# Kernel optimization log

Hardware: AMD Instinct MI355X
Metric: run time of the kernel (lower is better)

## Reference

```python
import jax, jax.numpy as jnp
import numpy as np

NUM_HEADS = 16
NUM_FEATURES = 1024
HEAD_DIM = NUM_FEATURES // NUM_HEADS
MAX_WAVELENGTH = 10000.0
SCALE_FACTOR = 1.0


def apply_rope(x, positions):
    # x: [B, S, H, D], positions: [B, S]
    half = HEAD_DIM // 2
    fraction = 2.0 * jnp.arange(half, dtype=x.dtype) / HEAD_DIM
    timescale = MAX_WAVELENGTH ** fraction                      # [half]
    sinusoid = positions[..., None].astype(x.dtype) / timescale  # [B, S, half]
    sinusoid = sinusoid[..., None, :] / SCALE_FACTOR             # [B, S, 1, half]
    sin, cos = jnp.sin(sinusoid), jnp.cos(sinusoid)
    x1, x2 = jnp.split(x, 2, axis=-1)
    return jnp.concatenate([x1 * cos - x2 * sin, x2 * cos + x1 * sin], axis=-1).astype(x.dtype)


def setup_inputs() -> dict:
    key = jax.random.key(0)
    ks = jax.random.split(key, 9)
    B, S, F = 2, 2048, NUM_FEATURES
    std = 1.0 / np.sqrt(F)
    inp = {
        "x": jax.random.normal(ks[0], (B, S, F), dtype=jnp.float32),
        "positions": jnp.broadcast_to(jnp.arange(S, dtype=jnp.int32), (B, S)),
        "Wq": jax.random.normal(ks[1], (F, F), dtype=jnp.float32) * std,
        "bq": jnp.zeros((F,), dtype=jnp.float32),
        "Wk": jax.random.normal(ks[2], (F, F), dtype=jnp.float32) * std,
        "bk": jnp.zeros((F,), dtype=jnp.float32),
        "Wv": jax.random.normal(ks[3], (F, F), dtype=jnp.float32) * std,
        "bv": jnp.zeros((F,), dtype=jnp.float32),
        "Wo": jax.random.normal(ks[4], (F, F), dtype=jnp.float32) * std,
        "bo": jnp.zeros((F,), dtype=jnp.float32),
    }
    return inp


def reference(x, positions, Wq, bq, Wk, bk, Wv, bv, Wo, bo):
    B, S, F = x.shape
    H, D = NUM_HEADS, HEAD_DIM
    q = (x @ Wq + bq).reshape(B, S, H, D)
    k = (x @ Wk + bk).reshape(B, S, H, D)
    v = (x @ Wv + bv).reshape(B, S, H, D)
    q = apply_rope(q, positions)
    k = apply_rope(k, positions)
    scale = jnp.sqrt(jnp.asarray(D, dtype=x.dtype))
    # scores: [B, H, S, S]
    scores = jnp.einsum("bqhd,bkhd->bhqk", q, k) / scale
    causal = jnp.tril(jnp.ones((S, S), dtype=bool))
    big_neg = jnp.finfo(scores.dtype).min
    scores = jnp.where(causal, scores, big_neg)
    attn = jax.nn.softmax(scores, axis=-1)
    out = jnp.einsum("bhqk,bkhd->bqhd", attn, v).reshape(B, S, F)
    return out @ Wo + bo
```

## Files before the change

kernel.cpp:

```cpp
#include <hip/hip_runtime.h>
#include <hip/hip_bf16.h>

#define S_LEN 2048
#define NF 1024
#define NH 16
#define HD 64
#define NB 2
#define M_TOT 4096

typedef __bf16 bf16x8 __attribute__((ext_vector_type(8)));
typedef float f32x4 __attribute__((ext_vector_type(4)));
typedef unsigned short u16;

__device__ __forceinline__ u16 f2bf(float f) {
  union { float f; unsigned u; } v; v.f = f;
  unsigned r = v.u + 0x7FFFu + ((v.u >> 16) & 1u);
  return (u16)(r >> 16);
}

__device__ __forceinline__ unsigned pk2bf(float a, float b) {
  __hip_bfloat162 t = __float22bfloat162_rn(make_float2(a, b));
  union { __hip_bfloat162 h; unsigned u; } u; u.h = t; return u.u;
}

__device__ __forceinline__ f32x4 mfma16(bf16x8 a, bf16x8 b, f32x4 c) {
  return __builtin_amdgcn_mfma_f32_16x16x32_bf16(a, b, c, 0, 0, 0);
}

__device__ __forceinline__ void gll16(const u16* g, u16* l) {
  __builtin_amdgcn_global_load_lds(
      (const __attribute__((address_space(1))) unsigned int*)g,
      (__attribute__((address_space(3))) unsigned int*)l, 16, 0, 0);
}

__device__ __forceinline__ u16* swz(u16* base, int row, int chunk) {
  return (u16*)((char*)base + row * 128 + ((chunk ^ (row & 7)) * 16));
}
__device__ __forceinline__ const u16* swz(const u16* base, int row, int chunk) {
  return (const u16*)((const char*)base + row * 128 + ((chunk ^ (row & 7)) * 16));
}

__global__ void __launch_bounds__(256) prep_kernel(
    const float* __restrict__ x, u16* __restrict__ xb,
    const int* __restrict__ positions, float2* __restrict__ rtab,
    const float* __restrict__ W0, const float* __restrict__ W1,
    const float* __restrict__ W2, const float* __restrict__ W3,
    u16* __restrict__ T0, u16* __restrict__ T1,
    u16* __restrict__ T2, u16* __restrict__ T3) {
  __shared__ float t[32][33];
  const int bx = blockIdx.x, tid = threadIdx.x;
  if (bx < 4096) {
    int i = (bx * 256 + tid) * 4;
    float4 v = *(const float4*)(x + i);
    ushort4 o;
    o.x = f2bf(v.x); o.y = f2bf(v.y); o.z = f2bf(v.z); o.w = f2bf(v.w);
    *(ushort4*)(xb + i) = o;
  } else if (bx < 4608) {
    int idx = (bx - 4096) * 256 + tid;
    int p = idx & 31;
    int bs = idx >> 5;
    float pos = (float)positions[bs];
    float ang = pos / __powf(10000.0f, (float)p * (1.0f / 32.0f));
    float sn, cs;
    sincosf(ang, &sn, &cs);
    rtab[idx] = make_float2(sn, cs);
  } else {
    int idx = bx - 4608;
    int z = idx >> 10, rem = idx & 1023;
    const float* W = (z == 0) ? W0 : (z == 1) ? W1 : (z == 2) ? W2 : W3;
    u16* Wt = (z == 0) ? T0 : (z == 1) ? T1 : (z == 2) ? T2 : T3;
    int n0 = (rem & 31) * 32, k0 = (rem >> 5) * 32;
    int tx = tid & 31, ty0 = tid >> 5;
#pragma unroll
    for (int i = 0; i < 4; i++) {
      int ty = ty0 + i * 8;
      t[ty][tx] = W[(size_t)(k0 + ty) * NF + n0 + tx];
    }
    __syncthreads();
#pragma unroll
    for (int i = 0; i < 4; i++) {
      int ty = ty0 + i * 8;
      Wt[(size_t)(n0 + ty) * NF + k0 + tx] = f2bf(t[tx][ty]);
    }
  }
}

__device__ __forceinline__ void mm_core(const u16* __restrict__ A, const u16* __restrict__ Bt,
                                        int m0, int n0, int kstart,
                                        u16* As, u16* Bs, f32x4 acc[4][4]) {
  const int tid = threadIdx.x;
  const int lane = tid & 63, w = tid >> 6;
  const int l15 = lane & 15, quad = lane >> 4;
  const int wr = w >> 1, wc = w & 1;
#pragma unroll
  for (int i = 0; i < 4; i++)
#pragma unroll
    for (int j = 0; j < 4; j++) {
      f32x4 z = {0.f, 0.f, 0.f, 0.f};
      acc[i][j] = z;
    }
  const u16* gA[4];
  const u16* gB[4];
#pragma unroll
  for (int i = 0; i < 4; i++) {
    int ci = i * 256 + tid;
    int row = ci >> 3, col = (ci & 7) ^ (row & 7);
    gA[i] = &A[(size_t)(m0 + row) * NF + col * 8];
    gB[i] = &Bt[(size_t)(n0 + row) * NF + col * 8];
  }
  for (int s = 0; s < NF / 64; s++) {
    const int k0 = ((s + kstart) & (NF / 64 - 1)) * 64;
    __syncthreads();
#pragma unroll
    for (int i = 0; i < 4; i++) {
      gll16(gA[i] + k0, &As[(i * 256 + w * 64) * 8]);
      gll16(gB[i] + k0, &Bs[(i * 256 + w * 64) * 8]);
    }
    __syncthreads();
#pragma unroll
    for (int kk = 0; kk < 2; kk++) {
      bf16x8 af[4], bfr[4];
#pragma unroll
      for (int i = 0; i < 4; i++)
        af[i] = *(const bf16x8*)swz(As, wr * 64 + i * 16 + l15, kk * 4 + quad);
#pragma unroll
      for (int j = 0; j < 4; j++)
        bfr[j] = *(const bf16x8*)swz(Bs, wc * 64 + j * 16 + l15, kk * 4 + quad);
#pragma unroll
      for (int i = 0; i < 4; i++)
#pragma unroll
        for (int j = 0; j < 4; j++)
          acc[i][j] = mfma16(af[i], bfr[j], acc[i][j]);
    }
  }
}

#define QSCL 0.18033688f

__global__ void __launch_bounds__(256) gemm_qkv_kernel(
    const u16* __restrict__ xb,
    const u16* __restrict__ wtq, const u16* __restrict__ wtk, const u16* __restrict__ wtv,
    const float* __restrict__ bq, const float* __restrict__ bk, const float* __restrict__ bv,
    const float2* __restrict__ rtab,
    u16* __restrict__ qo, u16* __restrict__ ko, u16* __restrict__ vto) {
  __shared__ u16 As[128 * 64], Bs[128 * 64];
  const int bx = blockIdx.x;
  const int xcd = bx & 7, slot = bx >> 3;
  const int z = slot >> 5, intra = slot & 31;
  const int by = (xcd >> 1) * 8 + (intra >> 2);
  const int bxn = (xcd & 1) * 4 + (intra & 3);
  const int kstart = (intra * 3 + z * 5) & 15;
  const u16* Wt = (z == 0) ? wtq : (z == 1) ? wtk : wtv;
  const float* bias = (z == 0) ? bq : (z == 1) ? bk : bv;
  const int m0 = by * 128, n0 = bxn * 128;
  f32x4 acc[4][4];
  mm_core(xb, Wt, m0, n0, kstart, As, Bs, acc);
  const int tid = threadIdx.x;
  const int lane = tid & 63, w = tid >> 6;
  const int l15 = lane & 15, quad = lane >> 4;
  const int wr = w >> 1, wc = w & 1;
  if (z < 2) {
    u16* out = (z == 0) ? qo : ko;
    const float oscl = (z == 0) ? QSCL : 1.0f;
#pragma unroll
    for (int i = 0; i < 4; i++) {
#pragma unroll
      for (int r = 0; r < 4; r++) {
        int gm = m0 + wr * 64 + i * 16 + quad * 4 + r;
        int b = gm >> 11, s = gm & 2047;
#pragma unroll
        for (int j = 0; j < 2; j++) {
          int col1 = n0 + wc * 64 + j * 16 + l15;
          int p = j * 16 + l15;
          float2 sc = rtab[gm * 32 + p];
          float x1 = acc[i][j][r] + bias[col1];
          float x2 = acc[i][j + 2][r] + bias[col1 + 32];
          float o1 = (x1 * sc.y - x2 * sc.x) * oscl;
          float o2 = (x2 * sc.y + x1 * sc.x) * oscl;
          int h = col1 >> 6;
          size_t base = ((size_t)((b * NH + h) * S_LEN + s)) * HD;
          out[base + p] = f2bf(o1);
          out[base + p + 32] = f2bf(o2);
        }
      }
    }
  } else {
#pragma unroll
    for (int i = 0; i < 4; i++) {
      int gm0 = m0 + wr * 64 + i * 16 + quad * 4;
      int b = gm0 >> 11, s0 = gm0 & 2047;
#pragma unroll
      for (int j = 0; j < 4; j++) {
        int col = n0 + wc * 64 + j * 16 + l15;
        int h = col >> 6, d = col & 63;
        float bb = bias[col];
        ushort4 pk;
        pk.x = f2bf(acc[i][j][0] + bb);
        pk.y = f2bf(acc[i][j][1] + bb);
        pk.z = f2bf(acc[i][j][2] + bb);
        pk.w = f2bf(acc[i][j][3] + bb);
        *(ushort4*)&vto[((size_t)((b * NH + h) * HD + d)) * S_LEN + s0] = pk;
      }
    }
  }
}

__global__ void __launch_bounds__(256) gemm_o_kernel(const u16* __restrict__ ab,
                                                     const u16* __restrict__ wto,
                                                     const float* __restrict__ bo,
                                                     float* __restrict__ out) {
  __shared__ u16 As[128 * 64], Bs[128 * 64];
  const int bxr = blockIdx.x;
  const int xcd = bxr & 7, intra = bxr >> 3;
  const int by = (xcd >> 1) * 8 + (intra >> 2);
  const int bxn = (xcd & 1) * 4 + (intra & 3);
  const int kstart = (intra * 3) & 15;
  const int m0 = by * 128, n0 = bxn * 128;
  f32x4 acc[4][4];
  mm_core(ab, wto, m0, n0, kstart, As, Bs, acc);
  const int tid = threadIdx.x;
  const int lane = tid & 63, w = tid >> 6;
  const int l15 = lane & 15, quad = lane >> 4;
  const int wr = w >> 1, wc = w & 1;
#pragma unroll
  for (int i = 0; i < 4; i++) {
#pragma unroll
    for (int j = 0; j < 4; j++) {
      int col = n0 + wc * 64 + j * 16 + l15;
      float bb = bo[col];
#pragma unroll
      for (int r = 0; r < 4; r++) {
        int gm = m0 + wr * 64 + i * 16 + quad * 4 + r;
        out[(size_t)gm * NF + col] = acc[i][j][r] + bb;
      }
    }
  }
}

__global__ void __launch_bounds__(256) attn_kernel(
    const u16* __restrict__ qb, const u16* __restrict__ kb,
    const u16* __restrict__ vtb, u16* __restrict__ ob) {
  __shared__ u16 ks[2 * 64 * 64];
  __shared__ u16 vs[2 * 64 * 64];
  __shared__ u16 ps[4][16 * 64];
  const int bx = blockIdx.x;
  const int qt = (bx < 512) ? (31 - (bx >> 5)) : ((bx - 512) >> 5);
  const int bh = bx & 31;
  const int tid = threadIdx.x;
  const int lane = tid & 63, w = tid >> 6, l15 = lane & 15, quad = lane >> 4;
  const int bb = bh >> 4, h = bh & 15;
  const size_t kvbase = (size_t)bh * S_LEN;
  const size_t vbase = (size_t)bh * HD;
  const int Q0 = qt * 64;
  const int nit = qt + 1;
  const int r0 = tid >> 3, c0 = tid & 7;
  const int r1 = r0 + 32;

  bf16x8 ones;
#pragma unroll
  for (int i = 0; i < 8; i++) ones[i] = (__bf16)1.0f;

  bf16x8 qf[2];
  {
    const u16* qrow = &qb[(kvbase + Q0 + w * 16 + l15) * HD];
#pragma unroll
    for (int hh = 0; hh < 2; hh++)
      qf[hh] = *(const bf16x8*)&qrow[hh * 32 + quad * 8];
  }

  float mrun = -1e30f;
  f32x4 Oa[4], lacc;
  { f32x4 z = {0.f, 0.f, 0.f, 0.f}; lacc = z;
#pragma unroll
    for (int t = 0; t < 4; t++) Oa[t] = z; }

  *(uint4*)swz(ks, r0, c0) = *(const uint4*)&kb[(kvbase + r0) * HD + c0 * 8];
  *(uint4*)swz(ks, r1, c0) = *(const uint4*)&kb[(kvbase + r1) * HD + c0 * 8];
  *(uint4*)swz(vs, r0, c0) = *(const uint4*)&vtb[(vbase + r0) * S_LEN + c0 * 8];
  *(uint4*)swz(vs, r1, c0) = *(const uint4*)&vtb[(vbase + r1) * S_LEN + c0 * 8];
  __syncthreads();

  int cur = 0;
  for (int it = 0; it < nit; ++it) {
    const int k0 = it * 64;
    const bool pf = (it + 1 < nit);
    u16* ksc = ks + cur * 4096;
    u16* vsc = vs + cur * 4096;
    uint4 pk0, pk1, pv0, pv1;
    if (pf) {
      int k1 = k0 + 64;
      pk0 = *(const uint4*)&kb[(kvbase + k1 + r0) * HD + c0 * 8];
      pk1 = *(const uint4*)&kb[(kvbase + k1 + r1) * HD + c0 * 8];
      pv0 = *(const uint4*)&vtb[(vbase + r0) * S_LEN + k1 + c0 * 8];
      pv1 = *(const uint4*)&vtb[(vbase + r1) * S_LEN + k1 + c0 * 8];
    }
    f32x4 sf[4];
#pragma unroll
    for (int t = 0; t < 4; t++) {
      bf16x8 ak0 = *(const bf16x8*)swz(ksc, t * 16 + l15, quad);
      bf16x8 ak1 = *(const bf16x8*)swz(ksc, t * 16 + l15, 4 + quad);
      f32x4 z = {0.f, 0.f, 0.f, 0.f};
      z = mfma16(ak0, qf[0], z);
      z = mfma16(ak1, qf[1], z);
      sf[t] = z;
    }
    if (it == qt) {
      int qg = Q0 + w * 16 + l15;
#pragma unroll
      for (int t = 0; t < 4; t++)
#pragma unroll
        for (int rr = 0; rr < 4; rr++)
          if (k0 + t * 16 + quad * 4 + rr > qg) sf[t][rr] = -1e30f;
    }
    float alph;
    {
      float mx = sf[0][0];
#pragma unroll
      for (int t = 0; t < 4; t++)
#pragma unroll
        for (int rr = 0; rr < 4; rr++) mx = fmaxf(mx, sf[t][rr]);
      mx = fmaxf(mx, __shfl_xor(mx, 16, 64));
      mx = fmaxf(mx, __shfl_xor(mx, 32, 64));
      float mnew = fmaxf(mrun, mx);
      alph = __builtin_amdgcn_exp2f(mrun - mnew);
      mrun = mnew;
#pragma unroll
      for (int t = 0; t < 4; t++)
#pragma unroll
        for (int rr = 0; rr < 4; rr++)
          sf[t][rr] = __builtin_amdgcn_exp2f(sf[t][rr] - mnew);
    }
    if (__any(alph < 1.f)) {
#pragma unroll
      for (int rr = 0; rr < 4; rr++) {
        float ao = __shfl(alph, quad * 4 + rr, 64);
#pragma unroll
        for (int t = 0; t < 4; t++) Oa[t][rr] *= ao;
        lacc[rr] *= ao;
      }
    }
#pragma unroll
    for (int t = 0; t < 4; t++) {
      uint2 pkk;
      pkk.x = pk2bf(sf[t][0], sf[t][1]);
      pkk.y = pk2bf(sf[t][2], sf[t][3]);
      int chnk = 2 * t + (quad >> 1);
      *(uint2*)((char*)ps[w] + l15 * 128 + ((chnk ^ (l15 & 7)) * 16) + (quad & 1) * 8) = pkk;
    }
    __builtin_amdgcn_wave_barrier();
    bf16x8 ap[2];
#pragma unroll
    for (int hh = 0; hh < 2; hh++)
      ap[hh] = *(const bf16x8*)swz(ps[w], l15, hh * 4 + quad);
#pragma unroll
    for (int t = 0; t < 4; t++) {
      bf16x8 bv0 = *(const bf16x8*)swz(vsc, t * 16 + l15, quad);
      bf16x8 bv1 = *(const bf16x8*)swz(vsc, t * 16 + l15, 4 + quad);
      Oa[t] = mfma16(ap[0], bv0, Oa[t]);
      Oa[t] = mfma16(ap[1], bv1, Oa[t]);
    }
    lacc = mfma16(ap[0], ones, lacc);
    lacc = mfma16(ap[1], ones, lacc);
    if (pf) {
      u16* ksn = ks + (cur ^ 1) * 4096;
      u16* vsn = vs + (cur ^ 1) * 4096;
      *(uint4*)swz(ksn, r0, c0) = pk0;
      *(uint4*)swz(ksn, r1, c0) = pk1;
      *(uint4*)swz(vsn, r0, c0) = pv0;
      *(uint4*)swz(vsn, r1, c0) = pv1;
      __syncthreads();
      cur ^= 1;
    }
  }

#pragma unroll
  for (int rr = 0; rr < 4; rr++) {
    float inv = 1.f / lacc[rr];
    int qg = Q0 + w * 16 + quad * 4 + rr;
    size_t rowb = ((size_t)(bb * S_LEN + qg)) * NF + h * HD;
#pragma unroll
    for (int t = 0; t < 4; t++)
      ob[rowb + t * 16 + l15] = f2bf(Oa[t][rr] * inv);
  }
}

extern "C" void kernel_launch(void* const* d_in, const int* in_sizes, int n_in,
                              void* d_out, int out_size, void* d_ws, size_t ws_size,
                              hipStream_t stream) {
  const float* x  = (const float*)d_in[0];
  const int* pos  = (const int*)d_in[1];
  const float* Wq = (const float*)d_in[2];
  const float* bq = (const float*)d_in[3];
  const float* Wk = (const float*)d_in[4];
  const float* bk = (const float*)d_in[5];
  const float* Wv = (const float*)d_in[6];
  const float* bv = (const float*)d_in[7];
  const float* Wo = (const float*)d_in[8];
  const float* bo = (const float*)d_in[9];
  float* out = (float*)d_out;

  u16* xb  = (u16*)d_ws;
  u16* wtq = xb + (size_t)M_TOT * NF;
  u16* wtk = wtq + (size_t)NF * NF;
  u16* wtv = wtk + (size_t)NF * NF;
  u16* wto = wtv + (size_t)NF * NF;
  u16* qb  = wto + (size_t)NF * NF;
  u16* kb  = qb + (size_t)M_TOT * NF;
  u16* vtb = kb + (size_t)M_TOT * NF;
  float2* rtab = (float2*)(vtb + (size_t)M_TOT * NF);
  u16* attnb = xb;

  prep_kernel<<<dim3(8704), 256, 0, stream>>>(x, xb, pos, rtab,
                                              Wq, Wk, Wv, Wo, wtq, wtk, wtv, wto);
  gemm_qkv_kernel<<<dim3(768), 256, 0, stream>>>(xb, wtq, wtk, wtv, bq, bk, bv,
                                                 rtab, qb, kb, vtb);
  attn_kernel<<<dim3(1024), 256, 0, stream>>>(qb, kb, vtb, attnb);
  gemm_o_kernel<<<dim3(256), 256, 0, stream>>>(attnb, wto, bo, out);
}
```

Baseline: 198.8 us.

## Use direct global-to-LDS loads in attention and 64-row tiles for output GEMM

The attention kernel now prefetches K and V tiles with direct global-to-LDS loads (gll16) into the spare buffer, replacing the register staging followed by swizzled LDS stores. The XOR swizzle moves into the global source address. The output projection GEMM switches to 64x128 tiles with a new mm_core64 routine, doubling the grid to 512 blocks so more CUs are filled. Risks: the direct LDS writes rely on the barrier placement for correctness, and the smaller GEMM tiles reuse less data per block.

```diff
diff --git a/kernel.cpp b/kernel.cpp
--- a/kernel.cpp
+++ b/kernel.cpp
@@ -135,6 +135,62 @@
   }
 }
 
+__device__ __forceinline__ void mm_core64(const u16* __restrict__ A, const u16* __restrict__ Bt,
+                                          int m0, int n0, int kstart,
+                                          u16* As, u16* Bs, f32x4 acc[2][4]) {
+  const int tid = threadIdx.x;
+  const int lane = tid & 63, w = tid >> 6;
+  const int l15 = lane & 15, quad = lane >> 4;
+  const int wr = w >> 1, wc = w & 1;
+#pragma unroll
+  for (int i = 0; i < 2; i++)
+#pragma unroll
+    for (int j = 0; j < 4; j++) {
+      f32x4 z = {0.f, 0.f, 0.f, 0.f};
+      acc[i][j] = z;
+    }
+  const u16* gA[2];
+  const u16* gB[4];
+#pragma unroll
+  for (int i = 0; i < 2; i++) {
+    int ci = i * 256 + tid;
+    int row = ci >> 3, col = (ci & 7) ^ (row & 7);
+    gA[i] = &A[(size_t)(m0 + row) * NF + col * 8];
+  }
+#pragma unroll
+  for (int i = 0; i < 4; i++) {
+    int ci = i * 256 + tid;
+    int row = ci >> 3, col = (ci & 7) ^ (row & 7);
+    gB[i] = &Bt[(size_t)(n0 + row) * NF + col * 8];
+  }
+  for (int s = 0; s < NF / 64; s++) {
+    const int k0 = ((s + kstart) & (NF / 64 - 1)) * 64;
+    __syncthreads();
+#pragma unroll
+    for (int i = 0; i < 2; i++)
+      gll16(gA[i] + k0, &As[(i * 256 + w * 64) * 8]);
+#pragma unroll
+    for (int i = 0; i < 4; i++)
+      gll16(gB[i] + k0, &Bs[(i * 256 + w * 64) * 8]);
+    __syncthreads();
+#pragma unroll
+    for (int kk = 0; kk < 2; kk++) {
+      bf16x8 af[2], bfr[4];
+#pragma unroll
+      for (int i = 0; i < 2; i++)
+        af[i] = *(const bf16x8*)swz(As, wr * 32 + i * 16 + l15, kk * 4 + quad);
+#pragma unroll
+      for (int j = 0; j < 4; j++)
+        bfr[j] = *(const bf16x8*)swz(Bs, wc * 64 + j * 16 + l15, kk * 4 + quad);
+#pragma unroll
+      for (int i = 0; i < 2; i++)
+#pragma unroll
+        for (int j = 0; j < 4; j++)
+          acc[i][j] = mfma16(af[i], bfr[j], acc[i][j]);
+    }
+  }
+}
+
 #define QSCL 0.18033688f
 
 __global__ void __launch_bounds__(256) gemm_qkv_kernel(
@@ -209,28 +265,28 @@
                                                      const u16* __restrict__ wto,
                                                      const float* __restrict__ bo,
                                                      float* __restrict__ out) {
-  __shared__ u16 As[128 * 64], Bs[128 * 64];
+  __shared__ u16 As[64 * 64], Bs[128 * 64];
   const int bxr = blockIdx.x;
   const int xcd = bxr & 7, intra = bxr >> 3;
-  const int by = (xcd >> 1) * 8 + (intra >> 2);
-  const int bxn = (xcd & 1) * 4 + (intra & 3);
+  const int by = xcd * 8 + (intra >> 3);
+  const int bxn = intra & 7;
   const int kstart = (intra * 3) & 15;
-  const int m0 = by * 128, n0 = bxn * 128;
-  f32x4 acc[4][4];
-  mm_core(ab, wto, m0, n0, kstart, As, Bs, acc);
+  const int m0 = by * 64, n0 = bxn * 128;
+  f32x4 acc[2][4];
+  mm_core64(ab, wto, m0, n0, kstart, As, Bs, acc);
   const int tid = threadIdx.x;
   const int lane = tid & 63, w = tid >> 6;
   const int l15 = lane & 15, quad = lane >> 4;
   const int wr = w >> 1, wc = w & 1;
 #pragma unroll
-  for (int i = 0; i < 4; i++) {
+  for (int i = 0; i < 2; i++) {
 #pragma unroll
     for (int j = 0; j < 4; j++) {
       int col = n0 + wc * 64 + j * 16 + l15;
       float bb = bo[col];
 #pragma unroll
       for (int r = 0; r < 4; r++) {
-        int gm = m0 + wr * 64 + i * 16 + quad * 4 + r;
+        int gm = m0 + wr * 32 + i * 16 + quad * 4 + r;
         out[(size_t)gm * NF + col] = acc[i][j][r] + bb;
       }
     }
@@ -253,8 +309,17 @@
   const size_t vbase = (size_t)bh * HD;
   const int Q0 = qt * 64;
   const int nit = qt + 1;
-  const int r0 = tid >> 3, c0 = tid & 7;
-  const int r1 = r0 + 32;
+
+  size_t kSrc[2], vSrc[2];
+  int dstOff[2];
+#pragma unroll
+  for (int i = 0; i < 2; i++) {
+    int ci = i * 256 + w * 64 + lane;
+    int kr = ci >> 3, kc = ci & 7;
+    kSrc[i] = (kvbase + kr) * HD + ((kc ^ (kr & 7)) * 8);
+    vSrc[i] = (vbase + kr) * S_LEN + ((kc ^ (kr & 7)) * 8);
+    dstOff[i] = (i * 256 + w * 64) * 8;
+  }
 
   bf16x8 ones;
 #pragma unroll
@@ -274,10 +339,11 @@
 #pragma unroll
     for (int t = 0; t < 4; t++) Oa[t] = z; }
 
-  *(uint4*)swz(ks, r0, c0) = *(const uint4*)&kb[(kvbase + r0) * HD + c0 * 8];
-  *(uint4*)swz(ks, r1, c0) = *(const uint4*)&kb[(kvbase + r1) * HD + c0 * 8];
-  *(uint4*)swz(vs, r0, c0) = *(const uint4*)&vtb[(vbase + r0) * S_LEN + c0 * 8];
-  *(uint4*)swz(vs, r1, c0) = *(const uint4*)&vtb[(vbase + r1) * S_LEN + c0 * 8];
+#pragma unroll
+  for (int i = 0; i < 2; i++) {
+    gll16(&kb[kSrc[i]], ks + dstOff[i]);
+    gll16(&vtb[vSrc[i]], vs + dstOff[i]);
+  }
   __syncthreads();
 
   int cur = 0;
@@ -286,13 +352,15 @@
     const bool pf = (it + 1 < nit);
     u16* ksc = ks + cur * 4096;
     u16* vsc = vs + cur * 4096;
-    uint4 pk0, pk1, pv0, pv1;
     if (pf) {
       int k1 = k0 + 64;
-      pk0 = *(const uint4*)&kb[(kvbase + k1 + r0) * HD + c0 * 8];
-      pk1 = *(const uint4*)&kb[(kvbase + k1 + r1) * HD + c0 * 8];
-      pv0 = *(const uint4*)&vtb[(vbase + r0) * S_LEN + k1 + c0 * 8];
-      pv1 = *(const uint4*)&vtb[(vbase + r1) * S_LEN + k1 + c0 * 8];
+      u16* ksn = ks + (cur ^ 1) * 4096;
+      u16* vsn = vs + (cur ^ 1) * 4096;
+#pragma unroll
+      for (int i = 0; i < 2; i++) {
+        gll16(&kb[kSrc[i] + (size_t)k1 * HD], ksn + dstOff[i]);
+        gll16(&vtb[vSrc[i] + k1], vsn + dstOff[i]);
+      }
     }
     f32x4 sf[4];
 #pragma unroll
@@ -362,12 +430,6 @@
     lacc = mfma16(ap[0], ones, lacc);
     lacc = mfma16(ap[1], ones, lacc);
     if (pf) {
-      u16* ksn = ks + (cur ^ 1) * 4096;
-      u16* vsn = vs + (cur ^ 1) * 4096;
-      *(uint4*)swz(ksn, r0, c0) = pk0;
-      *(uint4*)swz(ksn, r1, c0) = pk1;
-      *(uint4*)swz(vsn, r0, c0) = pv0;
-      *(uint4*)swz(vsn, r1, c0) = pv1;
       __syncthreads();
       cur ^= 1;
     }
@@ -415,5 +477,5 @@
   gemm_qkv_kernel<<<dim3(768), 256, 0, stream>>>(xb, wtq, wtk, wtv, bq, bk, bv,
                                                  rtab, qb, kb, vtb);
   attn_kernel<<<dim3(1024), 256, 0, stream>>>(qb, kb, vtb, attnb);
-  gemm_o_kernel<<<dim3(256), 256, 0, stream>>>(attnb, wto, bo, out);
-}
+  gemm_o_kernel<<<dim3(512), 256, 0, stream>>>(attnb, wto, bo, out);
+}
```

After: 194.2 us. -2.3%, faster.
